# Kernel tuning notes

Hardware: AMD Instinct MI355X
Metric: run time of the kernel (lower is better)

The kernel has to match this reference:

```python
import jax, jax.numpy as jnp
import numpy as np

NUM_SPECIAL = 3  # rows 1..NUM_SPECIAL in special table; row 0 is padding (zeros)

def setup_inputs() -> dict:
    key = jax.random.key(0)
    ks = jax.random.split(key, 16)
    T, B, E, H, L, V = 128, 32, 512, 512, 2, 32000
    G = 4 * H
    s = 0.02
    special_emb = jax.random.normal(ks[1], (NUM_SPECIAL + 1, E), jnp.float32) * s
    special_emb = special_emb.at[0].set(0.0)  # padding_idx=0
    return {
        "ids": jax.random.randint(ks[0], (T, B), 0, V),
        "length_countdown": jax.random.uniform(ks[2], (T, B, 1), jnp.float32),
        "word_emb": jax.random.normal(ks[3], (V, E), jnp.float32) * s,
        "special_emb": special_emb,
        "h0": jax.random.normal(ks[4], (L, B, H), jnp.float32) * s,
        "c0": jax.random.normal(ks[5], (L, B, H), jnp.float32) * s,
        "prev_output": jnp.zeros((B, H), jnp.float32),
        "Wih0": jax.random.normal(ks[6], (G, E + H + 1), jnp.float32) * s,
        "Whh0": jax.random.normal(ks[7], (G, H), jnp.float32) * s,
        "bih0": jnp.zeros((G,), jnp.float32),
        "bhh0": jnp.zeros((G,), jnp.float32),
        "Wih1": jax.random.normal(ks[8], (G, H), jnp.float32) * s,
        "Whh1": jax.random.normal(ks[9], (G, H), jnp.float32) * s,
        "bih1": jnp.zeros((G,), jnp.float32),
        "bhh1": jnp.zeros((G,), jnp.float32),
        "Wg": jax.random.normal(ks[10], (V, H), jnp.float32) * s,
        "bg": jnp.zeros((V,), jnp.float32),
    }

def _lstm_cell(x, h, c, Wih, Whh, bih, bhh):
    gates = x @ Wih.T + bih + h @ Whh.T + bhh  # [B, 4H]
    i, f, g, o = jnp.split(gates, 4, axis=-1)  # torch LSTMCell gate order
    c_new = jax.nn.sigmoid(f) * c + jax.nn.sigmoid(i) * jnp.tanh(g)
    h_new = jax.nn.sigmoid(o) * jnp.tanh(c_new)
    return h_new, c_new

def reference(ids, length_countdown, word_emb, special_emb, h0, c0, prev_output,
              Wih0, Whh0, bih0, bhh0, Wih1, Whh1, bih1, bhh1, Wg, bg):
    # embeddings = word_embeddings(ids) + special_embeddings(special_ids(ids))
    sp_ids = jnp.where(ids < NUM_SPECIAL, ids + 1, 0)
    emb = word_emb[ids] + special_emb[sp_ids]                 # [T,B,E]
    rnn_in = jnp.concatenate([emb, length_countdown], axis=2)  # [T,B,E+1]

    Wihs = (Wih0, Wih1); Whhs = (Whh0, Whh1)
    bihs = (bih0, bih1); bhhs = (bhh0, bhh1)
    L = h0.shape[0]

    def step(carry, emb_t):
        out, h, c = carry
        x = jnp.concatenate([emb_t, out], axis=1)  # input feeding
        hs, cs = [], []
        for l in range(L):
            h_l, c_l = _lstm_cell(x, h[l], c[l], Wihs[l], Whhs[l], bihs[l], bhhs[l])
            x = h_l  # dropout=0
            hs.append(h_l); cs.append(c_l)
        out = x
        score = jax.nn.log_softmax(out @ Wg.T + bg, axis=-1)  # generator
        return (out, jnp.stack(hs), jnp.stack(cs)), score

    (out, hT, cT), scores = jax.lax.scan(step, (prev_output, h0, c0), rnn_in)
    return scores, (hT, cT), out
```

## Files before the change

### kernel.cpp

```cpp
#include <hip/hip_runtime.h>
#include <hip/hip_bf16.h>


typedef __attribute__((ext_vector_type(8))) short bf16x8;
typedef __attribute__((ext_vector_type(4))) float f32x4;
typedef __attribute__((ext_vector_type(2))) unsigned long long u64x2;

#define AS1 __attribute__((address_space(1)))
#define AS3 __attribute__((address_space(3)))
#define RLX __ATOMIC_RELAXED
#define AGT __HIP_MEMORY_SCOPE_AGENT
#define NGEN 192
#define NSUB 32

__device__ __forceinline__ unsigned short f2bf(float f) {
  unsigned int u = __builtin_bit_cast(unsigned int, f);
  u += 0x7fffu + ((u >> 16) & 1u);
  return (unsigned short)(u >> 16);
}

__device__ __forceinline__ float bf2f(unsigned short us) {
  return __builtin_bit_cast(float, ((unsigned int)us) << 16);
}

__device__ __forceinline__ void gl16(const void* g, void* l) {
  __builtin_amdgcn_global_load_lds((const AS1 unsigned int*)g,
                                   (AS3 unsigned int*)l, 16, 0, 0);
}

__device__ __forceinline__ float sigm(float x) { return 1.0f / (1.0f + __expf(-x)); }

__global__ __launch_bounds__(256, 1) void prep_k(
    const float* __restrict__ Wg,  const float* __restrict__ Wih0,
    const float* __restrict__ Whh0,const float* __restrict__ Wih1,
    const float* __restrict__ Whh1,const float* __restrict__ bih0,
    const float* __restrict__ bhh0,const float* __restrict__ bih1,
    const float* __restrict__ bhh1,const float* __restrict__ h0,
    const float* __restrict__ pout,
    unsigned short* __restrict__ WgBf, unsigned short* __restrict__ W0e,
    unsigned short* __restrict__ Wr0p, unsigned short* __restrict__ Wr1p,
    float* __restrict__ b1p, float* __restrict__ bias0c,
    float* __restrict__ wcd, unsigned short* __restrict__ H0X,
    unsigned short* __restrict__ FOUT, unsigned short* __restrict__ H1I)
{
  const long N0 = 16384000L;
  const long N1 = N0 + 1048576L;
  const long N2 = N1 + 2097152L;
  const long N3 = N2 + 2097152L;
  const long N4 = N3 + 2048L;
  const long N5 = N4 + 2048L;
  const long N6 = N5 + 2048L;
  const long N7 = N6 + 49152L;
  for (long i = blockIdx.x * 256L + threadIdx.x; i < N7; i += 256L * gridDim.x) {
    if (i < N0) {
      WgBf[i] = f2bf(Wg[i]);
    } else if (i < N1) {
      long k = i - N0; int g = (int)(k >> 9); int kk = (int)(k & 511);
      W0e[k] = f2bf(Wih0[g * 1025 + kk]);
    } else if (i < N2) {
      long k = i - N1; int gp = (int)(k >> 10); int kk = (int)(k & 1023);
      int j = gp >> 2, gate = gp & 3; int g = gate * 512 + j;
      float v = (kk < 512) ? Whh0[g * 512 + kk] : Wih0[g * 1025 + 513 + (kk - 512)];
      Wr0p[k] = f2bf(v);
    } else if (i < N3) {
      long k = i - N2; int gp = (int)(k >> 10); int kk = (int)(k & 1023);
      int j = gp >> 2, gate = gp & 3; int g = gate * 512 + j;
      float v = (kk < 512) ? Wih1[g * 512 + kk] : Whh1[g * 512 + (kk - 512)];
      Wr1p[k] = f2bf(v);
    } else if (i < N4) {
      int gp = (int)(i - N3); int j = gp >> 2, gate = gp & 3; int g = gate * 512 + j;
      b1p[gp] = bih1[g] + bhh1[g];
    } else if (i < N5) {
      int g = (int)(i - N4); bias0c[g] = bih0[g] + bhh0[g];
    } else if (i < N6) {
      int g = (int)(i - N5); wcd[g] = Wih0[g * 1025 + 512];
    } else {
      long k = i - N6;
      int sub = (int)(k >> 14);
      int e = (int)(k & 16383);
      int wgx = e >> 9, b = (e >> 4) & 31, jl = e & 15;
      int j = wgx * 16 + jl;
      float v = (sub == 0) ? h0[b * 512 + j]
              : (sub == 1) ? h0[16384 + b * 512 + j]
                           : pout[b * 512 + j];
      unsigned short* dst = (sub == 0) ? H0X : (sub == 1) ? H1I : FOUT;
      dst[e] = f2bf(v);
    }
  }
}

__global__ __launch_bounds__(256, 1) void emb_k(
    const int* __restrict__ ids, const float* __restrict__ wemb,
    const float* __restrict__ semb, unsigned short* __restrict__ ebf)
{
  const int tb = blockIdx.x;
  const int id = ids[tb];
  const int sp = (id < 3) ? (id + 1) : 0;
  const float* wr = wemb + (long)id * 512;
  const float* sr = semb + sp * 512;
  for (int i = threadIdx.x; i < 512; i += 256)
    ebf[tb * 512 + i] = f2bf(wr[i] + sr[i]);
}

__global__ __launch_bounds__(256, 1) void gemm_p0(
    const unsigned short* __restrict__ A,
    const unsigned short* __restrict__ B, int N,
    float* __restrict__ C,
    const float* __restrict__ e0, const float* __restrict__ e1,
    const float* __restrict__ e2)
{
  __shared__ unsigned short sA[4096];
  __shared__ unsigned short sB[4096];
  const int tid = threadIdx.x;
  const int l = tid & 63, w = tid >> 6;
  const int nb = N >> 7;
  const int bid = blockIdx.x;
  const int bm = bid / nb, bn = bid - bm * nb;

  const int u0 = w * 128 + l;
  const int u1 = u0 + 64;
  const int r0 = u0 >> 2, c0 = (u0 & 3) ^ (r0 & 3);
  const int r1 = u1 >> 2, c1 = (u1 & 3) ^ (r1 & 3);
  const unsigned short* ga0 = A + (long)(bm * 128 + r0) * 512 + c0 * 8;
  const unsigned short* ga1 = A + (long)(bm * 128 + r1) * 512 + c1 * 8;
  const unsigned short* gb0 = B + (long)(bn * 128 + r0) * 512 + c0 * 8;
  const unsigned short* gb1 = B + (long)(bn * 128 + r1) * 512 + c1 * 8;
  unsigned short* la0 = sA + (w * 2 + 0) * 512;
  unsigned short* la1 = sA + (w * 2 + 1) * 512;
  unsigned short* lb0 = sB + (w * 2 + 0) * 512;
  unsigned short* lb1 = sB + (w * 2 + 1) * 512;

  const int fr = l & 15, fc = l >> 4;
  const int wm = w >> 1, wn = w & 1;
  int aoff[4], boff[4];
#pragma unroll
  for (int mi = 0; mi < 4; ++mi) {
    int row = wm * 64 + mi * 16 + fr;
    aoff[mi] = row * 64 + ((fc ^ (row & 3)) * 16);
  }
#pragma unroll
  for (int ni = 0; ni < 4; ++ni) {
    int row = wn * 64 + ni * 16 + fr;
    boff[ni] = row * 64 + ((fc ^ (row & 3)) * 16);
  }

  f32x4 acc[4][4];
#pragma unroll
  for (int i = 0; i < 4; ++i)
#pragma unroll
    for (int jq = 0; jq < 4; ++jq) acc[i][jq] = (f32x4){0.f, 0.f, 0.f, 0.f};

  for (int kt = 0; kt < 16; ++kt) {
    __syncthreads();
    gl16(ga0 + kt * 32, la0);
    gl16(ga1 + kt * 32, la1);
    gl16(gb0 + kt * 32, lb0);
    gl16(gb1 + kt * 32, lb1);
    asm volatile("s_waitcnt vmcnt(0)" ::: "memory");
    __syncthreads();
    bf16x8 av[4], bv[4];
#pragma unroll
    for (int mi = 0; mi < 4; ++mi)
      av[mi] = *(const bf16x8*)((const char*)sA + aoff[mi]);
#pragma unroll
    for (int ni = 0; ni < 4; ++ni)
      bv[ni] = *(const bf16x8*)((const char*)sB + boff[ni]);
#pragma unroll
    for (int mi = 0; mi < 4; ++mi)
#pragma unroll
      for (int ni = 0; ni < 4; ++ni)
        acc[mi][ni] = __builtin_amdgcn_mfma_f32_16x16x32_bf16(av[mi], bv[ni], acc[mi][ni], 0, 0, 0);
  }

  const int mbase = bm * 128 + wm * 64;
  const int nbase = bn * 128 + wn * 64;
#pragma unroll
  for (int mi = 0; mi < 4; ++mi)
#pragma unroll
    for (int ni = 0; ni < 4; ++ni) {
      const int col = nbase + ni * 16 + fr;
#pragma unroll
      for (int r = 0; r < 4; ++r) {
        const int row = mbase + mi * 16 + fc * 4 + r;
        const int gp = ((row & 511) << 2) | (row >> 9);
        float v = acc[mi][ni][r] + e0[row] + e2[col] * e1[row];
        C[(long)gp * N + col] = v;
      }
    }
}

__global__ __launch_bounds__(256, 1) void lstm_seq(
    const unsigned short* __restrict__ Wr0p,
    const unsigned short* __restrict__ Wr1p,
    float* __restrict__ P0t, const float* __restrict__ b1p,
    const float* __restrict__ c0in,
    unsigned short* __restrict__ H0X, unsigned short* __restrict__ H1X,
    const unsigned short* __restrict__ FOUT, const unsigned short* __restrict__ H1I,
    unsigned short* __restrict__ outbf, float* __restrict__ outs,
    unsigned int* __restrict__ flagA, unsigned int* __restrict__ flagB,
    unsigned int* __restrict__ flagC, unsigned int* __restrict__ cntBM,
    unsigned int* __restrict__ rowTk,
    const unsigned short* __restrict__ WgBf, const float* __restrict__ bg)
{
  const int tid = threadIdx.x;
  __shared__ char smem[75264] __attribute__((aligned(16)));

  if (blockIdx.x < 32) {
    unsigned short* sx = (unsigned short*)smem;
    float (*sg)[65] = (float(*)[65])(smem + 65536);
    unsigned short (*sh)[16] = (unsigned short(*)[16])(smem + 73856);

    const int wg = blockIdx.x;
    const int l = tid & 63, w = tid >> 6;
    const int fr = l & 15, fc = l >> 4;
    const int b = tid & 31, jl0 = tid >> 5;
    const int sb = l >> 1, sjh = l & 1;

    float c0r[2], c1r[2], h0k[2], h1k[2];
#pragma unroll
    for (int jq = 0; jq < 2; ++jq) {
      c0r[jq] = c0in[b * 512 + wg * 16 + jl0 + jq * 8];
      c1r[jq] = c0in[16384 + b * 512 + wg * 16 + jl0 + jq * 8];
      h0k[jq] = 0.f; h1k[jq] = 0.f;
    }

    float b1v[8];
#pragma unroll
    for (int jq = 0; jq < 2; ++jq)
#pragma unroll
      for (int g = 0; g < 4; ++g)
        b1v[jq * 4 + g] = b1p[(wg * 16 + jl0 + jq * 8) * 4 + g];

    const char* sxb0 = (const char*)sx + fr * 2048;
    const char* sxb1 = (const char*)sx + (16 + fr) * 2048;
    const int xr = (fr & 7) << 4;
    const int wrow = (wg * 64 + w * 16 + fr) * 1024 + fc * 8;

    char* const sxw = (char*)sx + sb * 2048;
    const int sswz = (sb & 7) << 4;

#define STAGE2(srcp, half)                                                    \
  do {                                                                        \
    unsigned long long q0[8], q1[8];                                          \
    _Pragma("unroll")                                                         \
    for (int i = 0; i < 8; ++i) {                                             \
      int u = i * 256 + tid;                                                  \
      q0[i] = __hip_atomic_load((const unsigned long long*)(srcp) + u * 2,    \
                                RLX, AGT);                                    \
      q1[i] = __hip_atomic_load((const unsigned long long*)(srcp) + u * 2 + 1,\
                                RLX, AGT);                                    \
    }                                                                         \
    _Pragma("unroll")                                                         \
    for (int i = 0; i < 8; ++i) {                                             \
      int cb = (half) * 1024 + (i * 4 + w) * 32 + sjh * 16;                   \
      u64x2 v; v.x = q0[i]; v.y = q1[i];                                      \
      *(u64x2*)(sxw + (cb ^ sswz)) = v;                                       \
    }                                                                         \
  } while (0)

#define MFMA_HALF(Wp, k0, a0v, a1v)                                           \
  do {                                                                        \
    _Pragma("unroll")                                                         \
    for (int kt = (k0); kt < (k0) + 16; ++kt) {                               \
      bf16x8 bv = *(const bf16x8*)((Wp) + wrow + kt * 32);                    \
      bf16x8 x0 = *(const bf16x8*)(sxb0 + ((kt * 64 + fc * 16) ^ xr));        \
      bf16x8 x1 = *(const bf16x8*)(sxb1 + ((kt * 64 + fc * 16) ^ xr));        \
      a0v = __builtin_amdgcn_mfma_f32_16x16x32_bf16(x0, bv, a0v, 0, 0, 0);    \
      a1v = __builtin_amdgcn_mfma_f32_16x16x32_bf16(x1, bv, a1v, 0, 0, 0);    \
    }                                                                         \
  } while (0)

#define POLL(flags, tgt)                                                      \
  do {                                                                        \
    const unsigned int* fp = (flags) + ((l & 31) << 5);                       \
    for (;;) {                                                                \
      unsigned int f = __hip_atomic_load(fp, RLX, AGT);                       \
      if (__all((int)(f >= (unsigned int)(tgt)))) break;                      \
      __builtin_amdgcn_s_sleep(1);                                            \
    }                                                                         \
    asm volatile("" ::: "memory");                                            \
  } while (0)

    STAGE2(H0X, 0);
    __syncthreads();
    if (tid == 0)
      __hip_atomic_store(&flagB[wg << 5], 1u, RLX, AGT);

    for (int t = 0; t < 128; ++t) {
      float p0v[8];
#pragma unroll
      for (int jq = 0; jq < 2; ++jq)
#pragma unroll
        for (int g = 0; g < 4; ++g)
          p0v[jq * 4 + g] =
              P0t[(long)((wg * 16 + jl0 + jq * 8) * 4 + g) * 4096 + t * 32 + b];

      f32x4 accA0 = (f32x4){0.f, 0.f, 0.f, 0.f};
      f32x4 accA1 = (f32x4){0.f, 0.f, 0.f, 0.f};
      MFMA_HALF(Wr0p, 0, accA0, accA1);

      POLL(flagB, t + 1);
      if (t == 0) STAGE2(FOUT, 1); else STAGE2(H1X, 1);
      __syncthreads();
      MFMA_HALF(Wr0p, 16, accA0, accA1);
#pragma unroll
      for (int r = 0; r < 4; ++r) {
        sg[fc * 4 + r][w * 16 + fr] = accA0[r];
        sg[16 + fc * 4 + r][w * 16 + fr] = accA1[r];
      }
      __syncthreads();
#pragma unroll
      for (int jq = 0; jq < 2; ++jq) {
        const int jl = jl0 + jq * 8;
        float gi = sg[b][jl * 4 + 0] + p0v[jq * 4 + 0];
        float gf = sg[b][jl * 4 + 1] + p0v[jq * 4 + 1];
        float gg = sg[b][jl * 4 + 2] + p0v[jq * 4 + 2];
        float go = sg[b][jl * 4 + 3] + p0v[jq * 4 + 3];
        float cn = sigm(gf) * c0r[jq] + sigm(gi) * tanhf(gg);
        float hn = sigm(go) * tanhf(cn);
        c0r[jq] = cn; h0k[jq] = hn;
        sh[b][jl] = f2bf(hn);
      }
      __syncthreads();
      if (w == 0) {
        u64x2 v = *(const u64x2*)&sh[sb][sjh * 8];
        unsigned long long* dst =
            (unsigned long long*)(H0X + wg * 512 + sb * 16 + sjh * 8);
        __hip_atomic_store(dst,     v.x, RLX, AGT);
        __hip_atomic_store(dst + 1, v.y, RLX, AGT);
        asm volatile("s_waitcnt vmcnt(0)" ::: "memory");
        if (tid == 0)
          __hip_atomic_store(&flagA[wg << 5], (unsigned int)(t + 1), RLX, AGT);
      }

      f32x4 accB0 = (f32x4){0.f, 0.f, 0.f, 0.f};
      f32x4 accB1 = (f32x4){0.f, 0.f, 0.f, 0.f};
      if (t == 0) {
        STAGE2(H1I, 1);
        __syncthreads();
      }
      MFMA_HALF(Wr1p, 16, accB0, accB1);

      POLL(flagA, t + 1);
      STAGE2(H0X, 0);
      __syncthreads();
      MFMA_HALF(Wr1p, 0, accB0, accB1);
#pragma unroll
      for (int r = 0; r < 4; ++r) {
        sg[fc * 4 + r][w * 16 + fr] = accB0[r];
        sg[16 + fc * 4 + r][w * 16 + fr] = accB1[r];
      }
      __syncthreads();
#pragma unroll
      for (int jq = 0; jq < 2; ++jq) {
        const int jl = jl0 + jq * 8;
        float gi = sg[b][jl * 4 + 0] + b1v[jq * 4 + 0];
        float gf = sg[b][jl * 4 + 1] + b1v[jq * 4 + 1];
        float gg = sg[b][jl * 4 + 2] + b1v[jq * 4 + 2];
        float go = sg[b][jl * 4 + 3] + b1v[jq * 4 + 3];
        float cn = sigm(gf) * c1r[jq] + sigm(gi) * tanhf(gg);
        float hn = sigm(go) * tanhf(cn);
        c1r[jq] = cn; h1k[jq] = hn;
        sh[b][jl] = f2bf(hn);
      }
      __syncthreads();
      if (w == 0) {
        u64x2 v = *(const u64x2*)&sh[sb][sjh * 8];
        unsigned long long* dst =
            (unsigned long long*)(H1X + wg * 512 + sb * 16 + sjh * 8);
        __hip_atomic_store(dst,     v.x, RLX, AGT);
        __hip_atomic_store(dst + 1, v.y, RLX, AGT);
        asm volatile("s_waitcnt vmcnt(0)" ::: "memory");
        if (tid == 0)
          __hip_atomic_store(&flagB[wg << 5], (unsigned int)(t + 2), RLX, AGT);
      } else if (w == 1) {
        const unsigned long long* s = (const unsigned long long*)&sh[sb][sjh * 8];
        unsigned long long* dst =
            (unsigned long long*)(outbf + (t * 32 + sb) * 512 + wg * 16 + sjh * 8);
        __hip_atomic_store(dst,     s[0], RLX, AGT);
        __hip_atomic_store(dst + 1, s[1], RLX, AGT);
        asm volatile("s_waitcnt vmcnt(0)" ::: "memory");
        if (l == 0)
          __hip_atomic_store(&flagC[wg << 5], (unsigned int)(t + 1), RLX, AGT);
      }
    }
#undef STAGE2
#undef MFMA_HALF
#undef POLL

    float* hT = outs + 131072000;
    float* cT = outs + 131072000 + 32768;
    float* oT = outs + 131072000 + 65536;
#pragma unroll
    for (int jq = 0; jq < 2; ++jq) {
      const int j = wg * 16 + jl0 + jq * 8;
      hT[b * 512 + j] = h0k[jq];
      hT[16384 + b * 512 + j] = h1k[jq];
      cT[b * 512 + j] = c0r[jq];
      cT[16384 + b * 512 + j] = c1r[jq];
      oT[b * 512 + j] = h1k[jq];
    }
    return;
  }

  if (blockIdx.x < 32 + NGEN) {
    unsigned short* sA  = (unsigned short*)smem;
    unsigned short* sB0 = (unsigned short*)(smem + 8192);
    unsigned short* sB1 = (unsigned short*)(smem + 16384);
    float (*pmw)[2][2] = (float(*)[2][2])(smem + 24576);

    const int g = (int)blockIdx.x - 32;
    const int l = tid & 63, w = tid >> 6;
    const int fr = l & 15, fc = l >> 4;
    const int wm = w >> 1, wn = w & 1;

    unsigned short* lg = (unsigned short*)outs;

    const int u0 = w * 128 + l, u1 = u0 + 64;
    const int r0 = u0 >> 2, c0 = (u0 & 3) ^ (r0 & 3);
    const int r1 = u1 >> 2, c1 = (u1 & 3) ^ (r1 & 3);
    unsigned short* lb00 = sB0 + (w * 2 + 0) * 512;
    unsigned short* lb01 = sB0 + (w * 2 + 1) * 512;
    unsigned short* lb10 = sB1 + (w * 2 + 0) * 512;
    unsigned short* lb11 = sB1 + (w * 2 + 1) * 512;

    int aoff[4], boff[4];
#pragma unroll
    for (int mi = 0; mi < 4; ++mi) {
      int row = wm * 64 + mi * 16 + fr;
      aoff[mi] = row * 64 + ((fc ^ (row & 3)) * 16);
    }
#pragma unroll
    for (int ni = 0; ni < 4; ++ni) {
      int row = wn * 64 + ni * 16 + fr;
      boff[ni] = row * 64 + ((fc ^ (row & 3)) * 16);
    }

    for (int job = g; job < 4000; job += NGEN) {
      const int bm = job / 125, bn2 = job - bm * 125;
      const int bn = bn2 * 2;

      if (w == 0) {
        const unsigned int* fp = flagC + ((l & 31) << 5);
        const unsigned int tgt = (unsigned int)(4 * bm + 4);
        for (;;) {
          unsigned int f = __hip_atomic_load(fp, RLX, AGT);
          if (__all((int)(f >= tgt))) break;
          __builtin_amdgcn_s_sleep(16);
        }
        asm volatile("" ::: "memory");
      }
      __syncthreads();

      const unsigned short* Ab0 = outbf + (long)(bm * 128 + r0) * 512 + c0 * 8;
      const unsigned short* Ab1 = outbf + (long)(bm * 128 + r1) * 512 + c1 * 8;
      const unsigned short* g00 = WgBf + (long)(bn * 128 + r0) * 512 + c0 * 8;
      const unsigned short* g01 = WgBf + (long)(bn * 128 + r1) * 512 + c1 * 8;
      const unsigned short* g10 = WgBf + (long)((bn + 1) * 128 + r0) * 512 + c0 * 8;
      const unsigned short* g11 = WgBf + (long)((bn + 1) * 128 + r1) * 512 + c1 * 8;

      f32x4 ac0[4][4], ac1[4][4];
#pragma unroll
      for (int i = 0; i < 4; ++i)
#pragma unroll
        for (int jq = 0; jq < 4; ++jq) {
          ac0[i][jq] = (f32x4){0.f, 0.f, 0.f, 0.f};
          ac1[i][jq] = (f32x4){0.f, 0.f, 0.f, 0.f};
        }

      for (int kt = 0; kt < 16; ++kt) {
        __syncthreads();
        unsigned long long a0x = __hip_atomic_load((const unsigned long long*)(Ab0 + kt * 32),     RLX, AGT);
        unsigned long long a0y = __hip_atomic_load((const unsigned long long*)(Ab0 + kt * 32) + 1, RLX, AGT);
        unsigned long long a1x = __hip_atomic_load((const unsigned long long*)(Ab1 + kt * 32),     RLX, AGT);
        unsigned long long a1y = __hip_atomic_load((const unsigned long long*)(Ab1 + kt * 32) + 1, RLX, AGT);
        gl16(g00 + kt * 32, lb00);
        gl16(g01 + kt * 32, lb01);
        gl16(g10 + kt * 32, lb10);
        gl16(g11 + kt * 32, lb11);
        { u64x2 va; va.x = a0x; va.y = a0y; *(u64x2*)((char*)sA + u0 * 16) = va; }
        { u64x2 va; va.x = a1x; va.y = a1y; *(u64x2*)((char*)sA + u1 * 16) = va; }
        asm volatile("s_waitcnt vmcnt(0)" ::: "memory");
        __syncthreads();
        bf16x8 av[4];
#pragma unroll
        for (int mi = 0; mi < 4; ++mi)
          av[mi] = *(const bf16x8*)((const char*)sA + aoff[mi]);
#pragma unroll
        for (int ni = 0; ni < 4; ++ni) {
          bf16x8 bv0 = *(const bf16x8*)((const char*)sB0 + boff[ni]);
          bf16x8 bv1 = *(const bf16x8*)((const char*)sB1 + boff[ni]);
#pragma unroll
          for (int mi = 0; mi < 4; ++mi) {
            ac0[mi][ni] = __builtin_amdgcn_mfma_f32_16x16x32_bf16(av[mi], bv0, ac0[mi][ni], 0, 0, 0);
            ac1[mi][ni] = __builtin_amdgcn_mfma_f32_16x16x32_bf16(av[mi], bv1, ac1[mi][ni], 0, 0, 0);
          }
        }
      }

      const int mbase = bm * 128 + wm * 64;
#pragma unroll
      for (int tt = 0; tt < 2; ++tt) {
        f32x4 (*ac)[4] = (tt == 0) ? ac0 : ac1;
        const int nbase = (bn + tt) * 128 + wn * 64;
        float m2[4][4], s2[4][4];
#pragma unroll
        for (int mi = 0; mi < 4; ++mi)
#pragma unroll
          for (int r = 0; r < 4; ++r) { m2[mi][r] = -3.0e38f; s2[mi][r] = 0.f; }
#pragma unroll
        for (int mi = 0; mi < 4; ++mi)
#pragma unroll
          for (int ni = 0; ni < 4; ++ni) {
            const int col = nbase + ni * 16 + fr;
            const float bgc = bg[col];
#pragma unroll
            for (int r = 0; r < 4; ++r) {
              float v = ac[mi][ni][r] + bgc;
              ac[mi][ni][r] = v;
              __hip_atomic_store(&lg[(long)(mbase + mi * 16 + fc * 4 + r) * 64000L + col],
                                 f2bf(v), RLX, AGT);
              m2[mi][r] = fmaxf(m2[mi][r], v);
            }
          }
#pragma unroll
        for (int mi = 0; mi < 4; ++mi)
#pragma unroll
          for (int r = 0; r < 4; ++r)
#pragma unroll
            for (int s = 1; s < 16; s <<= 1)
              m2[mi][r] = fmaxf(m2[mi][r], __shfl_xor(m2[mi][r], s));
#pragma unroll
        for (int mi = 0; mi < 4; ++mi)
#pragma unroll
          for (int ni = 0; ni < 4; ++ni)
#pragma unroll
            for (int r = 0; r < 4; ++r)
              s2[mi][r] += __expf(ac[mi][ni][r] - m2[mi][r]);
#pragma unroll
        for (int mi = 0; mi < 4; ++mi)
#pragma unroll
          for (int r = 0; r < 4; ++r)
#pragma unroll
            for (int s = 1; s < 16; s <<= 1)
              s2[mi][r] += __shfl_xor(s2[mi][r], s);
        if (fr == 0) {
#pragma unroll
          for (int mi = 0; mi < 4; ++mi)
#pragma unroll
            for (int r = 0; r < 4; ++r) {
              const int rl = wm * 64 + mi * 16 + fc * 4 + r;
              pmw[rl][wn][0] = m2[mi][r];
              pmw[rl][wn][1] = s2[mi][r];
            }
        }
        __syncthreads();
        if (tid < 128) {
          float ma = pmw[tid][0][0], sa = pmw[tid][0][1];
          float mb = pmw[tid][1][0], sb2 = pmw[tid][1][1];
          float M = fmaxf(ma, mb);
          float S = sa * __expf(ma - M) + sb2 * __expf(mb - M);
          int q2 = 2 * (tid * 250 + bn + tt);
          unsigned long long* p = (unsigned long long*)
              (P0t + ((long)(q2 >> 7)) * 4096 + 128L * bm + (q2 & 127));
          float2 o; o.x = M; o.y = S;
          __hip_atomic_store(p, __builtin_bit_cast(unsigned long long, o), RLX, AGT);
        }
        __syncthreads();
      }
      asm volatile("s_waitcnt vmcnt(0)" ::: "memory");
      __syncthreads();
      if (tid == 0)
        __hip_atomic_fetch_add(&cntBM[bm << 5], 2u, RLX, AGT);
      __syncthreads();
    }
  }

  {
    float* red = (float*)smem;
    unsigned* rowsh = (unsigned*)(smem + 64);
    unsigned short* lg = (unsigned short*)outs;

    for (;;) {
      if (tid == 0)
        rowsh[0] = __hip_atomic_fetch_add(rowTk, 1u, RLX, AGT);
      __syncthreads();
      const unsigned row = rowsh[0];
      if (row >= 4096u) break;
      const int bm = (int)(row >> 7), rl = (int)(row & 127);

      if (tid == 0) {
        for (;;) {
          unsigned c = __hip_atomic_load(&cntBM[bm << 5], RLX, AGT);
          if (c >= 250u) break;
          __builtin_amdgcn_s_sleep(32);
        }
      }
      __syncthreads();
      asm volatile("" ::: "memory");

      float m = -3.0e38f, sm = 0.0f;
      if (tid < 250) {
        int q2 = 2 * (rl * 250 + tid);
        const unsigned long long* pp = (const unsigned long long*)
            (P0t + ((long)(q2 >> 7)) * 4096 + 128L * bm + (q2 & 127));
        unsigned long long q = __hip_atomic_load(pp, RLX, AGT);
        float2 f = __builtin_bit_cast(float2, q);
        m = f.x; sm = f.y;
      }
#pragma unroll
      for (int off = 32; off > 0; off >>= 1) {
        float mo = __shfl_down(m, off);
        float so = __shfl_down(sm, off);
        float mn = fmaxf(m, mo);
        sm = sm * __expf(m - mn) + so * __expf(mo - mn);
        m = mn;
      }
      if ((tid & 63) == 0) { red[tid >> 6] = m; red[4 + (tid >> 6)] = sm; }
      __syncthreads();
      if (tid == 0) {
        float M = red[0], S = red[4];
#pragma unroll
        for (int i = 1; i < 4; ++i) {
          float mn = fmaxf(M, red[i]);
          S = S * __expf(M - mn) + red[4 + i] * __expf(red[i] - mn);
          M = mn;
        }
        red[8] = M + __logf(S);
      }
      __syncthreads();
      const float lse = red[8];

      const unsigned long long* base =
          (const unsigned long long*)(lg + (long)row * 64000L);
      unsigned long long q[32];
#pragma unroll
      for (int rr = 0; rr < 31; ++rr)
        q[rr] = __hip_atomic_load(base + rr * 256 + tid, RLX, AGT);
      if (tid < 64)
        q[31] = __hip_atomic_load(base + 7936 + tid, RLX, AGT);
      asm volatile("s_waitcnt vmcnt(0)" ::: "memory");
      __syncthreads();

      float* pr = outs + (long)row * 32000L;
#pragma unroll
      for (int rr = 0; rr < 31; ++rr) {
        unsigned long long qq = q[rr];
        float4 v;
        v.x = bf2f((unsigned short)(qq      )) - lse;
        v.y = bf2f((unsigned short)(qq >> 16)) - lse;
        v.z = bf2f((unsigned short)(qq >> 32)) - lse;
        v.w = bf2f((unsigned short)(qq >> 48)) - lse;
        *(float4*)(pr + (rr * 256 + tid) * 4) = v;
      }
      if (tid < 64) {
        unsigned long long qq = q[31];
        float4 v;
        v.x = bf2f((unsigned short)(qq      )) - lse;
        v.y = bf2f((unsigned short)(qq >> 16)) - lse;
        v.z = bf2f((unsigned short)(qq >> 32)) - lse;
        v.w = bf2f((unsigned short)(qq >> 48)) - lse;
        *(float4*)(pr + (7936 + tid) * 4) = v;
      }
      __syncthreads();
    }
  }
}

extern "C" void kernel_launch(void* const* d_in, const int* in_sizes, int n_in,
                              void* d_out, int out_size, void* d_ws, size_t ws_size,
                              hipStream_t stream) {
  const int*   ids  = (const int*)d_in[0];
  const float* cd   = (const float*)d_in[1];
  const float* wemb = (const float*)d_in[2];
  const float* semb = (const float*)d_in[3];
  const float* h0   = (const float*)d_in[4];
  const float* c0   = (const float*)d_in[5];
  const float* pout = (const float*)d_in[6];
  const float* Wih0 = (const float*)d_in[7];
  const float* Whh0 = (const float*)d_in[8];
  const float* bih0 = (const float*)d_in[9];
  const float* bhh0 = (const float*)d_in[10];
  const float* Wih1 = (const float*)d_in[11];
  const float* Whh1 = (const float*)d_in[12];
  const float* bih1 = (const float*)d_in[13];
  const float* bhh1 = (const float*)d_in[14];
  const float* Wg   = (const float*)d_in[15];
  const float* bg   = (const float*)d_in[16];
  float* out = (float*)d_out;

  char* ws = (char*)d_ws;
  unsigned short* WgBf   = (unsigned short*)(ws);
  unsigned short* W0e    = (unsigned short*)(ws + 32768000);
  unsigned short* Wr0p   = (unsigned short*)(ws + 34865152);
  unsigned short* Wr1p   = (unsigned short*)(ws + 39059456);
  float*          b1p    = (float*)(ws + 43253760);
  float*          bias0c = (float*)(ws + 43261952);
  float*          wcd    = (float*)(ws + 43270144);
  unsigned short* embbf  = (unsigned short*)(ws + 43278336);
  unsigned short* outbf  = (unsigned short*)(ws + 47472640);
  float*          P0t    = (float*)(ws + 51666944);
  unsigned int*   flagA  = (unsigned int*)(ws + 85221376);
  unsigned int*   flagB  = (unsigned int*)(ws + 85225472);
  unsigned short* H0X    = (unsigned short*)(ws + 85229568);
  unsigned short* H1X    = (unsigned short*)(ws + 85262336);
  unsigned short* FOUT   = (unsigned short*)(ws + 85295104);
  unsigned short* H1I    = (unsigned short*)(ws + 85327872);
  unsigned int*   flagC  = (unsigned int*)(ws + 85360640);
  unsigned int*   cntBM  = (unsigned int*)(ws + 85364736);
  unsigned int*   rowTk  = (unsigned int*)(ws + 85368832);

  hipMemsetAsync((void*)flagA, 0, 8192, stream);
  hipMemsetAsync((void*)flagC, 0, 12288, stream);

  prep_k<<<8192, 256, 0, stream>>>(Wg, Wih0, Whh0, Wih1, Whh1,
                                   bih0, bhh0, bih1, bhh1, h0, pout,
                                   WgBf, W0e, Wr0p, Wr1p, b1p, bias0c, wcd,
                                   H0X, FOUT, H1I);

  emb_k<<<4096, 256, 0, stream>>>(ids, wemb, semb, embbf);

  gemm_p0<<<512, 256, 0, stream>>>(W0e, embbf, 4096, P0t, bias0c, wcd, cd);

  lstm_seq<<<32 + NGEN + NSUB, 256, 0, stream>>>(Wr0p, Wr1p, P0t, b1p, c0,
                                                 H0X, H1X, FOUT, H1I, outbf, out,
                                                 flagA, flagB, flagC, cntBM,
                                                 rowTk, WgBf, bg);
}
```

Before: 1.759 ms.

## Move log-softmax finalize into a separate kernel instead of in-kernel subscriber blocks

Removes the 32 subscriber blocks that polled per-row-block counters and normalized logits inside the persistent kernel. Those blocks become extra generator blocks, and the finalize step runs as its own 4096-block lse_fin kernel after lstm_seq. This drops the atomics, counter polling and vmcnt waits, and lets the generator write plain stores. The cost is that the finalize can no longer overlap with the recurrence and generator work, so it adds a serial tail plus one extra launch.

Measured after the change: 1.739 ms. About the same (-1.2%).

```diff
diff --git a/kernel.cpp b/kernel.cpp
--- a/kernel.cpp
+++ b/kernel.cpp
@@ -10,8 +10,7 @@
 #define AS3 __attribute__((address_space(3)))
 #define RLX __ATOMIC_RELAXED
 #define AGT __HIP_MEMORY_SCOPE_AGENT
-#define NGEN 192
-#define NSUB 32
+#define NGEN 224
 
 __device__ __forceinline__ unsigned short f2bf(float f) {
   unsigned int u = __builtin_bit_cast(unsigned int, f);
@@ -198,8 +197,7 @@
     const unsigned short* __restrict__ FOUT, const unsigned short* __restrict__ H1I,
     unsigned short* __restrict__ outbf, float* __restrict__ outs,
     unsigned int* __restrict__ flagA, unsigned int* __restrict__ flagB,
-    unsigned int* __restrict__ flagC, unsigned int* __restrict__ cntBM,
-    unsigned int* __restrict__ rowTk,
+    unsigned int* __restrict__ flagC,
     const unsigned short* __restrict__ WgBf, const float* __restrict__ bg)
 {
   const int tid = threadIdx.x;
@@ -403,7 +401,7 @@
     return;
   }
 
-  if (blockIdx.x < 32 + NGEN) {
+  {
     unsigned short* sA  = (unsigned short*)smem;
     unsigned short* sB0 = (unsigned short*)(smem + 8192);
     unsigned short* sB1 = (unsigned short*)(smem + 16384);
@@ -518,8 +516,7 @@
             for (int r = 0; r < 4; ++r) {
               float v = ac[mi][ni][r] + bgc;
               ac[mi][ni][r] = v;
-              __hip_atomic_store(&lg[(long)(mbase + mi * 16 + fc * 4 + r) * 64000L + col],
-                                 f2bf(v), RLX, AGT);
+              lg[(long)(mbase + mi * 16 + fc * 4 + r) * 64000L + col] = f2bf(v);
               m2[mi][r] = fmaxf(m2[mi][r], v);
             }
           }
@@ -561,109 +558,81 @@
           float M = fmaxf(ma, mb);
           float S = sa * __expf(ma - M) + sb2 * __expf(mb - M);
           int q2 = 2 * (tid * 250 + bn + tt);
-          unsigned long long* p = (unsigned long long*)
-              (P0t + ((long)(q2 >> 7)) * 4096 + 128L * bm + (q2 & 127));
-          float2 o; o.x = M; o.y = S;
-          __hip_atomic_store(p, __builtin_bit_cast(unsigned long long, o), RLX, AGT);
+          float* p = P0t + ((long)(q2 >> 7)) * 4096 + 128L * bm + (q2 & 127);
+          p[0] = M; p[1] = S;
         }
         __syncthreads();
       }
-      asm volatile("s_waitcnt vmcnt(0)" ::: "memory");
-      __syncthreads();
-      if (tid == 0)
-        __hip_atomic_fetch_add(&cntBM[bm << 5], 2u, RLX, AGT);
-      __syncthreads();
-    }
-  }
-
-  {
-    float* red = (float*)smem;
-    unsigned* rowsh = (unsigned*)(smem + 64);
-    unsigned short* lg = (unsigned short*)outs;
-
-    for (;;) {
-      if (tid == 0)
-        rowsh[0] = __hip_atomic_fetch_add(rowTk, 1u, RLX, AGT);
-      __syncthreads();
-      const unsigned row = rowsh[0];
-      if (row >= 4096u) break;
-      const int bm = (int)(row >> 7), rl = (int)(row & 127);
-
-      if (tid == 0) {
-        for (;;) {
-          unsigned c = __hip_atomic_load(&cntBM[bm << 5], RLX, AGT);
-          if (c >= 250u) break;
-          __builtin_amdgcn_s_sleep(32);
-        }
-      }
-      __syncthreads();
-      asm volatile("" ::: "memory");
-
-      float m = -3.0e38f, sm = 0.0f;
-      if (tid < 250) {
-        int q2 = 2 * (rl * 250 + tid);
-        const unsigned long long* pp = (const unsigned long long*)
-            (P0t + ((long)(q2 >> 7)) * 4096 + 128L * bm + (q2 & 127));
-        unsigned long long q = __hip_atomic_load(pp, RLX, AGT);
-        float2 f = __builtin_bit_cast(float2, q);
-        m = f.x; sm = f.y;
-      }
-#pragma unroll
-      for (int off = 32; off > 0; off >>= 1) {
-        float mo = __shfl_down(m, off);
-        float so = __shfl_down(sm, off);
-        float mn = fmaxf(m, mo);
-        sm = sm * __expf(m - mn) + so * __expf(mo - mn);
-        m = mn;
-      }
-      if ((tid & 63) == 0) { red[tid >> 6] = m; red[4 + (tid >> 6)] = sm; }
-      __syncthreads();
-      if (tid == 0) {
-        float M = red[0], S = red[4];
-#pragma unroll
-        for (int i = 1; i < 4; ++i) {
-          float mn = fmaxf(M, red[i]);
-          S = S * __expf(M - mn) + red[4 + i] * __expf(red[i] - mn);
-          M = mn;
-        }
-        red[8] = M + __logf(S);
-      }
-      __syncthreads();
-      const float lse = red[8];
-
-      const unsigned long long* base =
-          (const unsigned long long*)(lg + (long)row * 64000L);
-      unsigned long long q[32];
-#pragma unroll
-      for (int rr = 0; rr < 31; ++rr)
-        q[rr] = __hip_atomic_load(base + rr * 256 + tid, RLX, AGT);
-      if (tid < 64)
-        q[31] = __hip_atomic_load(base + 7936 + tid, RLX, AGT);
-      asm volatile("s_waitcnt vmcnt(0)" ::: "memory");
-      __syncthreads();
-
-      float* pr = outs + (long)row * 32000L;
-#pragma unroll
-      for (int rr = 0; rr < 31; ++rr) {
-        unsigned long long qq = q[rr];
-        float4 v;
-        v.x = bf2f((unsigned short)(qq      )) - lse;
-        v.y = bf2f((unsigned short)(qq >> 16)) - lse;
-        v.z = bf2f((unsigned short)(qq >> 32)) - lse;
-        v.w = bf2f((unsigned short)(qq >> 48)) - lse;
-        *(float4*)(pr + (rr * 256 + tid) * 4) = v;
-      }
-      if (tid < 64) {
-        unsigned long long qq = q[31];
-        float4 v;
-        v.x = bf2f((unsigned short)(qq      )) - lse;
-        v.y = bf2f((unsigned short)(qq >> 16)) - lse;
-        v.z = bf2f((unsigned short)(qq >> 32)) - lse;
-        v.w = bf2f((unsigned short)(qq >> 48)) - lse;
-        *(float4*)(pr + (7936 + tid) * 4) = v;
-      }
-      __syncthreads();
-    }
+    }
+  }
+}
+
+__global__ __launch_bounds__(256, 1) void lse_fin(float* __restrict__ sc,
+                                                  const float* __restrict__ pmsbase)
+{
+  __shared__ float red[9];
+  const long row = blockIdx.x;
+  const int bm = (int)(row >> 7), rl = (int)(row & 127);
+  const int tid = threadIdx.x;
+
+  float m = -3.0e38f, sm = 0.0f;
+  if (tid < 250) {
+    int q2 = 2 * (rl * 250 + tid);
+    const float* p = pmsbase + ((long)(q2 >> 7)) * 4096 + 128L * bm + (q2 & 127);
+    m = p[0]; sm = p[1];
+  }
+#pragma unroll
+  for (int off = 32; off > 0; off >>= 1) {
+    float mo = __shfl_down(m, off);
+    float so = __shfl_down(sm, off);
+    float mn = fmaxf(m, mo);
+    sm = sm * __expf(m - mn) + so * __expf(mo - mn);
+    m = mn;
+  }
+  if ((tid & 63) == 0) { red[tid >> 6] = m; red[4 + (tid >> 6)] = sm; }
+  __syncthreads();
+  if (tid == 0) {
+    float M = red[0], S = red[4];
+#pragma unroll
+    for (int i = 1; i < 4; ++i) {
+      float mn = fmaxf(M, red[i]);
+      S = S * __expf(M - mn) + red[4 + i] * __expf(red[i] - mn);
+      M = mn;
+    }
+    red[8] = M + __logf(S);
+  }
+  __syncthreads();
+  const float lse = red[8];
+
+  const unsigned long long* base =
+      (const unsigned long long*)((const unsigned short*)sc + row * 64000L);
+  unsigned long long q[32];
+#pragma unroll
+  for (int rr = 0; rr < 31; ++rr)
+    q[rr] = base[rr * 256 + tid];
+  if (tid < 64)
+    q[31] = base[7936 + tid];
+  __syncthreads();
+
+  float* pr = sc + row * 32000L;
+#pragma unroll
+  for (int rr = 0; rr < 31; ++rr) {
+    unsigned long long qq = q[rr];
+    float4 v;
+    v.x = bf2f((unsigned short)(qq      )) - lse;
+    v.y = bf2f((unsigned short)(qq >> 16)) - lse;
+    v.z = bf2f((unsigned short)(qq >> 32)) - lse;
+    v.w = bf2f((unsigned short)(qq >> 48)) - lse;
+    *(float4*)(pr + (rr * 256 + tid) * 4) = v;
+  }
+  if (tid < 64) {
+    unsigned long long qq = q[31];
+    float4 v;
+    v.x = bf2f((unsigned short)(qq      )) - lse;
+    v.y = bf2f((unsigned short)(qq >> 16)) - lse;
+    v.z = bf2f((unsigned short)(qq >> 32)) - lse;
+    v.w = bf2f((unsigned short)(qq >> 48)) - lse;
+    *(float4*)(pr + (7936 + tid) * 4) = v;
   }
 }
 
@@ -707,11 +676,9 @@
   unsigned short* FOUT   = (unsigned short*)(ws + 85295104);
   unsigned short* H1I    = (unsigned short*)(ws + 85327872);
   unsigned int*   flagC  = (unsigned int*)(ws + 85360640);
-  unsigned int*   cntBM  = (unsigned int*)(ws + 85364736);
-  unsigned int*   rowTk  = (unsigned int*)(ws + 85368832);
 
   hipMemsetAsync((void*)flagA, 0, 8192, stream);
-  hipMemsetAsync((void*)flagC, 0, 12288, stream);
+  hipMemsetAsync((void*)flagC, 0, 4096, stream);
 
   prep_k<<<8192, 256, 0, stream>>>(Wg, Wih0, Whh0, Wih1, Whh1,
                                    bih0, bhh0, bih1, bhh1, h0, pout,
@@ -722,8 +689,9 @@
 
   gemm_p0<<<512, 256, 0, stream>>>(W0e, embbf, 4096, P0t, bias0c, wcd, cd);
 
-  lstm_seq<<<32 + NGEN + NSUB, 256, 0, stream>>>(Wr0p, Wr1p, P0t, b1p, c0,
-                                                 H0X, H1X, FOUT, H1I, outbf, out,
-                                                 flagA, flagB, flagC, cntBM,
-                                                 rowTk, WgBf, bg);
-}
+  lstm_seq<<<32 + NGEN, 256, 0, stream>>>(Wr0p, Wr1p, P0t, b1p, c0,
+                                          H0X, H1X, FOUT, H1I, outbf, out,
+                                          flagA, flagB, flagC, WgBf, bg);
+
+  lse_fin<<<4096, 256, 0, stream>>>(out, P0t);
+}
```
